# Kernel optimization log

Measured on AMD Instinct MI355X. Metric: run time of the kernel, lower is better.

The kernel has to match this reference:

```python
import jax, jax.numpy as jnp
import numpy as np

L, H, HD = 2, 8, 256
B, SP, SS = 2, 1024, 256
DP, DE = 2048, 1024
FP, FE = 8192, 4096
S = SP + SS


def setup_inputs() -> dict:
    key = jax.random.key(0)
    ks = iter(jax.random.split(key, 40))

    def w(shape):
        return jax.random.normal(next(ks), shape, jnp.float32) * (shape[-2] ** -0.5)

    inp = {
        "emb_p": jax.random.normal(next(ks), (B, SP, DP), jnp.float32),
        "emb_e": jax.random.normal(next(ks), (B, SS, DE), jnp.float32),
        "cond_p": jax.random.normal(next(ks), (B, DP), jnp.float32),
        "cond_e": jax.random.normal(next(ks), (B, DE), jnp.float32),
        "p_ada1": w((L, DP, 2 * DP)),
        "p_ada2": w((L, DP, 2 * DP)),
        "p_adaF": w((DP, 2 * DP)),
        "p_wq": w((L, DP, H * HD)),
        "p_wk": w((L, DP, H * HD)),
        "p_wv": w((L, DP, H * HD)),
        "p_wo": w((L, H * HD, DP)),
        "p_wg": w((L, DP, FP)),
        "p_wu": w((L, DP, FP)),
        "p_wd": w((L, FP, DP)),
        "e_ada1": w((L, DE, 2 * DE)),
        "e_ada2": w((L, DE, 2 * DE)),
        "e_adaF": w((DE, 2 * DE)),
        "e_wq": w((L, DE, H * HD)),
        "e_wk": w((L, DE, H * HD)),
        "e_wv": w((L, DE, H * HD)),
        "e_wo": w((L, H * HD, DE)),
        "e_wg": w((L, DE, FE)),
        "e_wu": w((L, DE, FE)),
        "e_wd": w((L, FE, DE)),
        "position_ids": jnp.broadcast_to(jnp.arange(S, dtype=jnp.int32)[None], (B, S)),
        "attn_mask": jnp.ones((B, S, S), dtype=bool),
    }
    return inp


def _rms(x):
    return x * jax.lax.rsqrt(jnp.mean(x * x, axis=-1, keepdims=True) + 1e-6)


def _ada(x, cond, W):
    # AdaRMS: cond -> (scale, gate); normed = rms(x) * (1 + scale)
    scale, gate = jnp.split(cond @ W, 2, axis=-1)  # each [B, D]
    return _rms(x) * (1.0 + scale)[:, None, :], gate[:, None, :]


def _rot_half(x):
    a, b = jnp.split(x, 2, axis=-1)
    return jnp.concatenate([-b, a], axis=-1)


def _forward(emb_p, emb_e, cond_p, cond_e,
             p_ada1, p_ada2, p_adaF, p_wq, p_wk, p_wv, p_wo, p_wg, p_wu, p_wd,
             e_ada1, e_ada2, e_adaF, e_wq, e_wk, e_wv, e_wo, e_wg, e_wu, e_wd,
             position_ids, attn_mask):
    # RoPE tables [B, 1, S, HD]
    inv = 1.0 / (10000.0 ** (jnp.arange(0, HD, 2, dtype=jnp.float32) / HD))
    fr = position_ids.astype(jnp.float32)[..., None] * inv  # [B, S, HD/2]
    ang = jnp.concatenate([fr, fr], axis=-1)
    cos, sin = jnp.cos(ang)[:, None], jnp.sin(ang)[:, None]
    bias = jnp.where(attn_mask[:, None], 0.0, jnp.finfo(jnp.float32).min)  # [B,1,S,S]
    scaling = HD ** -0.5

    xs = [emb_p, emb_e]
    conds = [cond_p, cond_e]
    prm = [
        dict(a1=p_ada1, a2=p_ada2, wq=p_wq, wk=p_wk, wv=p_wv, wo=p_wo, wg=p_wg, wu=p_wu, wd=p_wd),
        dict(a1=e_ada1, a2=e_ada2, wq=e_wq, wk=e_wk, wv=e_wv, wo=e_wo, wg=e_wg, wu=e_wu, wd=e_wd),
    ]
    seq_lens = [SP, SS]

    def heads(y):
        return y.reshape(B, -1, H, HD).transpose(0, 2, 1, 3)

    for l in range(L):
        qs, ksl, vs, gates = [], [], [], []
        for i in range(2):
            p = prm[i]
            h, g = _ada(xs[i], conds[i], p["a1"][l])
            gates.append(g)
            qs.append(heads(h @ p["wq"][l]))
            ksl.append(heads(h @ p["wk"][l]))
            vs.append(heads(h @ p["wv"][l]))
        # joint streams concatenated along sequence
        q = jnp.concatenate(qs, axis=2)   # [B,H,S,HD]
        k = jnp.concatenate(ksl, axis=2)
        v = jnp.concatenate(vs, axis=2)
        q = q * cos + _rot_half(q) * sin
        k = k * cos + _rot_half(k) * sin
        scores = jnp.einsum("bhqd,bhkd->bhqk", q, k) * scaling + bias
        probs = jax.nn.softmax(scores, axis=-1)
        att = jnp.einsum("bhqk,bhkd->bhqd", probs, v)
        att = att.transpose(0, 2, 1, 3).reshape(B, S, H * HD)
        start = 0
        for i in range(2):
            p = prm[i]
            end = start + seq_lens[i]
            o = att[:, start:end] @ p["wo"][l]
            x = xs[i] + o * gates[i]                 # gated attention residual
            res = x
            h2, g2 = _ada(x, conds[i], p["a2"][l])
            m = (jax.nn.gelu(h2 @ p["wg"][l], approximate=True) * (h2 @ p["wu"][l])) @ p["wd"][l]
            xs[i] = res + m * g2                     # gated MLP residual
            start = end
    out_p, _ = _ada(xs[0], cond_p, p_adaF)
    out_e, _ = _ada(xs[1], cond_e, e_adaF)
    return out_p, out_e


def reference(emb_p, emb_e, cond_p, cond_e,
              p_ada1, p_ada2, p_adaF, p_wq, p_wk, p_wv, p_wo, p_wg, p_wu, p_wd,
              e_ada1, e_ada2, e_adaF, e_wq, e_wk, e_wv, e_wo, e_wg, e_wu, e_wd,
              position_ids, attn_mask):
    return _forward(emb_p, emb_e, cond_p, cond_e,
                    p_ada1, p_ada2, p_adaF, p_wq, p_wk, p_wv, p_wo, p_wg, p_wu, p_wd,
                    e_ada1, e_ada2, e_adaF, e_wq, e_wk, e_wv, e_wo, e_wg, e_wu, e_wd,
                    position_ids, attn_mask)
```

## Files before the change

### kernel.cpp

```cpp
#include <hip/hip_runtime.h>
#include <math.h>

namespace {

constexpr int NL = 2, NH = 8, DH = 256;
constexpr int NB = 2, SEQP = 1024, SEQS = 256, SEQ = SEQP + SEQS;
constexpr int DIMP = 2048, DIME = 1024, FFP = 8192, FFE = 4096;
constexpr int HH = NH * DH;
constexpr int QKVN = 3 * HH;

typedef __attribute__((ext_vector_type(8))) short bf16x8;
typedef __attribute__((ext_vector_type(4))) float f32x4;

__device__ inline ushort f2b(float f) {
  union { float f; unsigned u; } x{f};
  unsigned r = (x.u + 0x7FFFu + ((x.u >> 16) & 1u)) >> 16;
  return (ushort)r;
}
__device__ inline float b2f(ushort u) {
  union { unsigned u; float f; } x{(unsigned)u << 16};
  return x.f;
}
__device__ inline void stv(float* p, float v) { *p = v; }
__device__ inline void stv(ushort* p, float v) { *p = f2b(v); }

__device__ inline void gld16(const void* g, void* l) {
  __builtin_amdgcn_global_load_lds(
      (const __attribute__((address_space(1))) void*)g,
      (__attribute__((address_space(3))) void*)l, 16, 0, 0);
}


__global__ void copy4_k(float4* __restrict__ dst, const float4* __restrict__ src) {
  long i = (long)blockIdx.x * blockDim.x + threadIdx.x;
  dst[i] = src[i];
}

__global__ void rope_tab_k(const int* __restrict__ pos, float* __restrict__ cosb,
                           float* __restrict__ sinb) {
  long bs = blockIdx.x;
  int d = threadIdx.x;
  int i = d & (DH / 2 - 1);
  float inv = expf(-(2.0f * (float)i / (float)DH) * logf(10000.0f));
  float ang = (float)pos[bs] * inv;
  cosb[bs * DH + d] = cosf(ang);
  sinb[bs * DH + d] = sinf(ang);
}

__global__ __launch_bounds__(256) void ada_k(const float* __restrict__ cond,
    const float* __restrict__ W, float* __restrict__ part, int D, int twoD) {
  __shared__ float lc[2 * 2048];
  int t = threadIdx.x;
  int j = blockIdx.x * 256 + t;
  int chunk = blockIdx.y;
  int cl = D / gridDim.y;
  int d0 = chunk * cl;
  for (int i = t; i < 2 * D; i += 256) lc[i] = cond[i];
  __syncthreads();
  float a0 = 0.f, a1 = 0.f;
  for (int d = d0; d < d0 + cl; ++d) {
    float wvv = W[(long)d * twoD + j];
    a0 = fmaf(lc[d], wvv, a0);
    a1 = fmaf(lc[D + d], wvv, a1);
  }
  part[((long)chunk * 2 + 0) * twoD + j] = a0;
  part[((long)chunk * 2 + 1) * twoD + j] = a1;
}

__global__ void ada_red_k(const float* __restrict__ part, float* __restrict__ sg,
                          int twoD, int nch) {
  int idx = blockIdx.x * 256 + threadIdx.x;
  int b = idx / twoD, j = idx - b * twoD;
  float s = 0.f;
  for (int c = 0; c < nch; ++c) s += part[((long)c * 2 + b) * twoD + j];
  sg[(long)b * twoD + j] = s;
}

template <typename OT>
__global__ __launch_bounds__(256) void rms_k(const float* __restrict__ x,
    const float* __restrict__ sg, OT* __restrict__ out, int D, int rowsPerB) {
  long row = blockIdx.x;
  int b = (int)(row / rowsPerB);
  const float* xr = x + row * (long)D;
  OT* po = out + row * (long)D;
  const float* sc = sg + (long)b * 2 * D;
  int t = threadIdx.x;
  float ss = 0.f;
  for (int i = t; i < D; i += 256) { float v = xr[i]; ss = fmaf(v, v, ss); }
  for (int o = 32; o; o >>= 1) ss += __shfl_xor(ss, o);
  __shared__ float wr[4];
  if ((t & 63) == 0) wr[t >> 6] = ss;
  __syncthreads();
  float rs = rsqrtf((wr[0] + wr[1] + wr[2] + wr[3]) / (float)D + 1e-6f);
  for (int i = t; i < D; i += 256) stv(po + i, xr[i] * rs * (1.f + sc[i]));
}

__global__ void gated_add_k(float* __restrict__ x, const float* __restrict__ y,
                            const float* __restrict__ g, int D, int rowsPerB) {
  long idx = (long)blockIdx.x * 256 + threadIdx.x;
  int d = (int)(idx % D);
  int b = (int)(idx / ((long)rowsPerB * D));
  x[idx] = fmaf(y[idx], g[(long)b * 2 * D + d], x[idx]);
}

__global__ __launch_bounds__(256) void wconv_k(const float* __restrict__ in,
    ushort* __restrict__ out, int N, int K) {
  __shared__ float tile[64][65];
  int n0 = blockIdx.x << 6, k0 = blockIdx.y << 6;
  int t = threadIdx.x, r = t >> 4, c4 = (t & 15) << 2;
#pragma unroll
  for (int rr = 0; rr < 64; rr += 16) {
    float4 v = *(const float4*)(in + (long)(k0 + r + rr) * N + n0 + c4);
    tile[r + rr][c4 + 0] = v.x; tile[r + rr][c4 + 1] = v.y;
    tile[r + rr][c4 + 2] = v.z; tile[r + rr][c4 + 3] = v.w;
  }
  __syncthreads();
#pragma unroll
  for (int rr = 0; rr < 64; rr += 16) {
    int n = r + rr;
    ushort4 o;
    o.x = f2b(tile[c4 + 0][n]); o.y = f2b(tile[c4 + 1][n]);
    o.z = f2b(tile[c4 + 2][n]); o.w = f2b(tile[c4 + 3][n]);
    *(ushort4*)(out + (long)(n0 + n) * K + k0 + c4) = o;
  }
}

__global__ __launch_bounds__(256) void rope_qk_k(const ushort* __restrict__ qkv,
    const float* __restrict__ cosb, const float* __restrict__ sinb,
    ushort* __restrict__ qj, ushort* __restrict__ kj, int Si, int ofs) {
  long bs = blockIdx.x;
  int b = (int)(bs / Si), s = (int)(bs % Si);
  int c = blockIdx.y * 256 + threadIdx.x;
  int h = c >> 8, hd = c & 255;
  long tin = bs * (long)QKVN;
  float q = b2f(qkv[tin + c]), k = b2f(qkv[tin + HH + c]);
  float qp = b2f(qkv[tin + (c ^ 128)]), kp = b2f(qkv[tin + HH + (c ^ 128)]);
  long sgi = ((long)b * SEQ + ofs + s) * DH + hd;
  float cv = cosb[sgi], sv = sinb[sgi];
  float qr = (hd < 128) ? -qp : qp, kr = (hd < 128) ? -kp : kp;
  long o = (((long)b * NH + h) * SEQ + ofs + s) * (long)DH + hd;
  qj[o] = f2b(fmaf(q, cv, qr * sv));
  kj[o] = f2b(fmaf(k, cv, kr * sv));
}

__global__ __launch_bounds__(256) void vtrans_k(const ushort* __restrict__ qkv,
    ushort* __restrict__ vjT, int Si, int ofs) {
  __shared__ ushort tile[64][80];
  int z = blockIdx.z, b = z >> 3, h = z & 7;
  int s0 = blockIdx.x << 6, d0 = blockIdx.y << 6;
  int t = threadIdx.x, r = t >> 3, c8 = (t & 7) << 3;
#pragma unroll
  for (int rr = 0; rr < 64; rr += 32) {
    const ushort* src = qkv + (long)(b * Si + s0 + r + rr) * QKVN + 2 * HH + h * DH + d0 + c8;
    *(uint4*)&tile[r + rr][c8] = *(const uint4*)src;
  }
  __syncthreads();
#pragma unroll
  for (int rr = 0; rr < 64; rr += 32) {
    int drow = r + rr;
    ushort o[8];
#pragma unroll
    for (int j = 0; j < 8; ++j) o[j] = tile[c8 + j][drow];
    *(uint4*)(vjT + ((long)(b * NH + h) * DH + d0 + drow) * SEQ + ofs + s0 + c8) =
        *(const uint4*)o;
  }
}

__global__ __launch_bounds__(256) void softmax_k(float* __restrict__ scores) {
  float* p = scores + (long)blockIdx.y * SEQ * SEQ + (long)blockIdx.x * SEQ;
  ushort* po = (ushort*)p;
  int t = threadIdx.x;
  float v[5];
  float mx = -3.4e38f;
#pragma unroll
  for (int i = 0; i < 5; ++i) { v[i] = p[t + i * 256] * 0.0625f; mx = fmaxf(mx, v[i]); }
  for (int o = 32; o; o >>= 1) mx = fmaxf(mx, __shfl_xor(mx, o));
  __shared__ float wr[4];
  if ((t & 63) == 0) wr[t >> 6] = mx;
  __syncthreads();
  mx = fmaxf(fmaxf(wr[0], wr[1]), fmaxf(wr[2], wr[3]));
  __syncthreads();
  float s = 0.f;
#pragma unroll
  for (int i = 0; i < 5; ++i) { v[i] = expf(v[i] - mx); s += v[i]; }
  for (int o = 32; o; o >>= 1) s += __shfl_xor(s, o);
  if ((t & 63) == 0) wr[t >> 6] = s;
  __syncthreads();
  float inv = 1.f / (wr[0] + wr[1] + wr[2] + wr[3]);
#pragma unroll
  for (int i = 0; i < 5; ++i) po[t + i * 256] = f2b(v[i] * inv);
}

__global__ __launch_bounds__(256) void gelumul_k(const ushort* __restrict__ in,
    ushort* __restrict__ out, int F) {
  long v = (long)blockIdx.x * 256 + threadIdx.x;
  int fv = F >> 3;
  long m = v / fv; int f8 = (int)(v % fv) << 3;
  const ushort* gp = in + m * 2 * F + f8;
  uint4 gv = *(const uint4*)gp;
  uint4 uv = *(const uint4*)(gp + F);
  const ushort* gs = (const ushort*)&gv;
  const ushort* us = (const ushort*)&uv;
  ushort ov[8];
#pragma unroll
  for (int j = 0; j < 8; ++j) {
    float g = b2f(gs[j]);
    float ge = 0.5f * g * (1.f + tanhf(0.7978845608028654f * fmaf(0.044715f * g, g * g, g)));
    ov[j] = f2b(ge * b2f(us[j]));
  }
  *(uint4*)(out + m * F + f8) = *(const uint4*)ov;
}

__global__ void redsum_k(const float4* __restrict__ in, float4* __restrict__ out,
                         long MN4, int ns) {
  long i = (long)blockIdx.x * 256 + threadIdx.x;
  float4 s = in[i];
  for (int c = 1; c < ns; ++c) {
    float4 v = in[(long)c * MN4 + i];
    s.x += v.x; s.y += v.y; s.z += v.z; s.w += v.w;
  }
  out[i] = s;
}

template <int EPI>
__global__ __launch_bounds__(256) void bgemm_k(
    const ushort* __restrict__ A, const ushort* __restrict__ B,
    float* __restrict__ Cf, ushort* __restrict__ Cb, int K,
    int lda, int ldb, int ldc,
    long sA1, long sA2, long sB1, long sB2, long sC1, long sC2, int bdiv) {
  __shared__ ushort As[128 * 32];
  __shared__ ushort Bs[128 * 32];
  int t = threadIdx.x;
  int z = blockIdx.z, z1 = z / bdiv, z2 = z % bdiv;
  A += z1 * sA1 + z2 * sA2;
  B += z1 * sB1 + z2 * sB2;
  long cofs = z1 * sC1 + z2 * sC2;
  int m0 = blockIdx.y * 128, n0 = blockIdx.x * 128;
  int srow = t >> 2, scol = (t & 3) << 3;
  const ushort* gA0 = A + (long)(m0 + srow) * lda + scol;
  const ushort* gA1 = A + (long)(m0 + srow + 64) * lda + scol;
  const ushort* gB0 = B + (long)(n0 + srow) * ldb + scol;
  const ushort* gB1 = B + (long)(n0 + srow + 64) * ldb + scol;
  ushort* lA0 = &As[srow * 32 + scol];
  ushort* lA1 = &As[(srow + 64) * 32 + scol];
  ushort* lB0 = &Bs[srow * 32 + scol];
  ushort* lB1 = &Bs[(srow + 64) * 32 + scol];
  int lane = t & 63;
  int wm = ((t >> 6) & 1) << 6, wn = (t >> 7) << 6;
  int fr = lane & 15, fk = (lane >> 4) << 3;
  f32x4 acc[4][4] = {};
  for (int k0 = 0; k0 < K; k0 += 32) {
    if (k0) __syncthreads();
    gld16(gA0 + k0, lA0);
    gld16(gA1 + k0, lA1);
    gld16(gB0 + k0, lB0);
    gld16(gB1 + k0, lB1);
    __syncthreads();
    bf16x8 a[4], b[4];
#pragma unroll
    for (int m = 0; m < 4; ++m)
      a[m] = *(const bf16x8*)&As[(wm + m * 16 + fr) * 32 + fk];
#pragma unroll
    for (int n = 0; n < 4; ++n)
      b[n] = *(const bf16x8*)&Bs[(wn + n * 16 + fr) * 32 + fk];
#pragma unroll
    for (int m = 0; m < 4; ++m)
#pragma unroll
      for (int n = 0; n < 4; ++n)
        acc[m][n] = __builtin_amdgcn_mfma_f32_16x16x32_bf16(a[m], b[n], acc[m][n], 0, 0, 0);
  }
  int cr = (lane >> 4) << 2, cc = lane & 15;
#pragma unroll
  for (int m = 0; m < 4; ++m) {
    int row = m0 + wm + m * 16 + cr;
#pragma unroll
    for (int n = 0; n < 4; ++n) {
      int col = n0 + wn + n * 16 + cc;
#pragma unroll
      for (int r = 0; r < 4; ++r) {
        long idx = cofs + (long)(row + r) * ldc + col;
        if (EPI == 0) Cf[idx] = acc[m][n][r];
        else Cb[idx] = f2b(acc[m][n][r]);
      }
    }
  }
}

template <int EPI>
__global__ __launch_bounds__(512, 2) void bgemm256_k(
    const ushort* __restrict__ A, const ushort* __restrict__ B,
    float* __restrict__ Cf, ushort* __restrict__ Cb, int K,
    int lda, int ldb, int ldc,
    long sA1, long sA2, long sB1, long sB2, long sC1, long sC2, int bdiv) {
  __shared__ ushort As[4][256 * 32];
  __shared__ ushort Bs[4][256 * 32];
  int t = threadIdx.x;
  int z = blockIdx.z, z1 = z / bdiv, z2 = z % bdiv;
  A += z1 * sA1 + z2 * sA2;
  B += z1 * sB1 + z2 * sB2;
  long cofs = z1 * sC1 + z2 * sC2;
  int nx = gridDim.x;
  int nwg = nx * gridDim.y;
  int wg = blockIdx.y * nx + blockIdx.x;
  int q = nwg >> 3, r = nwg & 7;
  int xcd = wg & 7, wi = wg >> 3;
  int swz = (xcd < r ? xcd * (q + 1) : r * (q + 1) + (xcd - r) * q) + wi;
  int n0 = (swz % nx) << 8;
  int m0 = (swz / nx) << 8;

  int srow = t >> 2;
  int gc = ((t & 3) ^ ((srow >> 1) & 3)) << 3;
  const ushort* ga0 = A + (long)(m0 + srow) * lda + gc;
  const ushort* ga1 = A + (long)(m0 + 128 + srow) * lda + gc;
  const ushort* gb0 = B + (long)(n0 + srow) * ldb + gc;
  const ushort* gb1 = B + (long)(n0 + 128 + srow) * ldb + gc;

  int lane = t & 63, wid = t >> 6;
  int wm = wid >> 2, wn = wid & 3;
  int fr = lane & 15, sl = lane >> 4;

  int aoff[8], boff[4];
#pragma unroll
  for (int m = 0; m < 8; ++m) {
    int row = wm * 128 + m * 16 + fr;
    aoff[m] = row * 32 + ((sl ^ ((row >> 1) & 3)) << 3);
  }
#pragma unroll
  for (int n = 0; n < 4; ++n) {
    int row = wn * 64 + n * 16 + fr;
    boff[n] = row * 32 + ((sl ^ ((row >> 1) & 3)) << 3);
  }

  f32x4 acc[8][4] = {};
  int nt = K >> 5;

#define STAGE(ti) { int b_ = (ti) & 3; int k_ = (ti) << 5;        \
    gld16(ga0 + k_, &As[b_][t * 8]);                              \
    gld16(ga1 + k_, &As[b_][4096 + t * 8]);                       \
    gld16(gb0 + k_, &Bs[b_][t * 8]);                              \
    gld16(gb1 + k_, &Bs[b_][4096 + t * 8]); }

  STAGE(0); STAGE(1); STAGE(2);
  for (int ti = 0; ti < nt; ++ti) {
    if (ti + 2 < nt)      asm volatile("s_waitcnt vmcnt(8)" ::: "memory");
    else if (ti + 1 < nt) asm volatile("s_waitcnt vmcnt(4)" ::: "memory");
    else                  asm volatile("s_waitcnt vmcnt(0)" ::: "memory");
    __builtin_amdgcn_s_barrier();
    if (ti + 3 < nt) STAGE(ti + 3);
    int bu = ti & 3;
    bf16x8 av[8], bv[4];
#pragma unroll
    for (int m = 0; m < 8; ++m) av[m] = *(const bf16x8*)&As[bu][aoff[m]];
#pragma unroll
    for (int n = 0; n < 4; ++n) bv[n] = *(const bf16x8*)&Bs[bu][boff[n]];
    __builtin_amdgcn_s_setprio(1);
#pragma unroll
    for (int m = 0; m < 8; ++m)
#pragma unroll
      for (int n = 0; n < 4; ++n)
        acc[m][n] = __builtin_amdgcn_mfma_f32_16x16x32_bf16(av[m], bv[n], acc[m][n], 0, 0, 0);
    __builtin_amdgcn_s_setprio(0);
  }
#undef STAGE

  int cr = sl << 2, cc = fr;
#pragma unroll
  for (int m = 0; m < 8; ++m) {
    int row = m0 + wm * 128 + m * 16 + cr;
#pragma unroll
    for (int n = 0; n < 4; ++n) {
      int col = n0 + wn * 64 + n * 16 + cc;
#pragma unroll
      for (int rr = 0; rr < 4; ++rr) {
        long idx = cofs + (long)(row + rr) * ldc + col;
        if (EPI == 0) Cf[idx] = acc[m][n][rr];
        else Cb[idx] = f2b(acc[m][n][rr]);
      }
    }
  }
}

}

extern "C" void kernel_launch(void* const* d_in, const int* in_sizes, int n_in,
                              void* d_out, int out_size, void* d_ws, size_t ws_size,
                              hipStream_t stream) {
  (void)in_sizes; (void)n_in; (void)out_size;
  const float* emb_p = (const float*)d_in[0];
  const float* emb_e = (const float*)d_in[1];
  const float* cond[2] = {(const float*)d_in[2], (const float*)d_in[3]};
  const float* ada1[2] = {(const float*)d_in[4], (const float*)d_in[14]};
  const float* ada2[2] = {(const float*)d_in[5], (const float*)d_in[15]};
  const float* adaF[2] = {(const float*)d_in[6], (const float*)d_in[16]};
  const float* wq[2] = {(const float*)d_in[7], (const float*)d_in[17]};
  const float* wk[2] = {(const float*)d_in[8], (const float*)d_in[18]};
  const float* wv[2] = {(const float*)d_in[9], (const float*)d_in[19]};
  const float* wo[2] = {(const float*)d_in[10], (const float*)d_in[20]};
  const float* wg[2] = {(const float*)d_in[11], (const float*)d_in[21]};
  const float* wu[2] = {(const float*)d_in[12], (const float*)d_in[22]};
  const float* wd[2] = {(const float*)d_in[13], (const float*)d_in[23]};
  const int* pos = (const int*)d_in[24];

  const int Ds[2] = {DIMP, DIME};
  const int Fs[2] = {FFP, FFE};
  const int Sis[2] = {SEQP, SEQS};
  const int ofss[2] = {0, SEQP};

  char* base = (char*)d_ws;
  size_t off = 0;
  auto alF = [&](size_t n) { float* r = (float*)(base + off); off += (n * 4 + 255) & ~(size_t)255; return r; };
  auto alH = [&](size_t n) { ushort* r = (ushort*)(base + off); off += (n * 2 + 255) & ~(size_t)255; return r; };

  float* xs[2]; ushort* hb[2]; float* sg[2];
  xs[0] = alF((size_t)NB * SEQP * DIMP);
  xs[1] = alF((size_t)NB * SEQS * DIME);
  float* cosb = alF((size_t)NB * SEQ * DH);
  float* sinb = alF((size_t)NB * SEQ * DH);
  sg[0] = alF((size_t)NB * 2 * DIMP);
  sg[1] = alF((size_t)NB * 2 * DIME);
  float* part = alF((size_t)8 * 2 * 2 * DIMP);
  float* tmp = alF((size_t)NB * SEQP * DIMP);
  float* scores = alF((size_t)NB * NH * SEQ * SEQ);
  hb[0] = alH((size_t)NB * SEQP * DIMP);
  hb[1] = alH((size_t)NB * SEQS * DIME);
  ushort* qkvt = alH((size_t)NB * SEQP * QKVN);
  ushort* qj = alH((size_t)NB * NH * SEQ * DH);
  ushort* kj = alH((size_t)NB * NH * SEQ * DH);
  ushort* vjT = alH((size_t)NB * NH * DH * SEQ);
  ushort* att2b = alH((size_t)NB * SEQ * HH);
  ushort* wT = alH((size_t)2 * FFP * DIMP);
  if (off > ws_size) return;

  float* pbuf = scores;
  ushort* ffb2 = (ushort*)scores;
  ushort* ffb = (ushort*)((char*)scores + (size_t)70 * 1024 * 1024);

  copy4_k<<<(NB * SEQP * DIMP / 4) / 256, 256, 0, stream>>>((float4*)xs[0], (const float4*)emb_p);
  copy4_k<<<(NB * SEQS * DIME / 4) / 256, 256, 0, stream>>>((float4*)xs[1], (const float4*)emb_e);
  rope_tab_k<<<NB * SEQ, DH, 0, stream>>>(pos, cosb, sinb);

  for (int l = 0; l < NL; ++l) {
    for (int i = 0; i < 2; ++i) {
      int D = Ds[i], Si = Sis[i], M = NB * Si;
      const float* a1 = ada1[i] + (size_t)l * D * 2 * D;
      ada_k<<<dim3(2 * D / 256, 8), 256, 0, stream>>>(cond[i], a1, part, D, 2 * D);
      ada_red_k<<<4 * D / 256, 256, 0, stream>>>(part, sg[i], 2 * D, 8);
      rms_k<ushort><<<M, 256, 0, stream>>>(xs[i], sg[i], hb[i], D, Si);
      const float* W3[3] = {wq[i] + (size_t)l * D * HH, wk[i] + (size_t)l * D * HH,
                            wv[i] + (size_t)l * D * HH};
      for (int j = 0; j < 3; ++j)
        wconv_k<<<dim3(HH / 64, D / 64), 256, 0, stream>>>(W3[j], wT + (size_t)j * HH * D, HH, D);
      if (i == 0)
        bgemm256_k<1><<<dim3(QKVN / 256, M / 256, 1), 512, 0, stream>>>(
            hb[i], wT, nullptr, qkvt, D, D, D, QKVN, 0, 0, 0, 0, 0, 0, 1);
      else
        bgemm_k<1><<<dim3(QKVN / 128, M / 128, 1), 256, 0, stream>>>(
            hb[i], wT, nullptr, qkvt, D, D, D, QKVN, 0, 0, 0, 0, 0, 0, 1);
      rope_qk_k<<<dim3(M, HH / 256), 256, 0, stream>>>(qkvt, cosb, sinb, qj, kj, Si, ofss[i]);
      vtrans_k<<<dim3(Si / 64, DH / 64, NB * NH), 256, 0, stream>>>(qkvt, vjT, Si, ofss[i]);
    }
    bgemm256_k<0><<<dim3(SEQ / 256, SEQ / 256, NB * NH), 512, 0, stream>>>(
        qj, kj, scores, nullptr, DH, DH, DH, SEQ,
        (long)SEQ * DH, 0, (long)SEQ * DH, 0, (long)SEQ * SEQ, 0, 1);
    softmax_k<<<dim3(SEQ, NB * NH), 256, 0, stream>>>(scores);
    bgemm_k<1><<<dim3(DH / 128, SEQ / 128, NB * NH), 256, 0, stream>>>(
        (const ushort*)scores, vjT, nullptr, att2b, SEQ, 2 * SEQ, SEQ, HH,
        (long)2 * NH * SEQ * SEQ, (long)2 * SEQ * SEQ,
        (long)NH * DH * SEQ, (long)DH * SEQ,
        (long)SEQ * HH, (long)DH, NH);
    for (int i = 0; i < 2; ++i) {
      int D = Ds[i], F = Fs[i], Si = Sis[i], M = NB * Si;
      wconv_k<<<dim3(D / 64, HH / 64), 256, 0, stream>>>(wo[i] + (size_t)l * HH * D, wT, D, HH);
      if (i == 0)
        bgemm256_k<0><<<dim3(D / 256, Si / 256, NB * 4), 512, 0, stream>>>(
            att2b, wT, pbuf, nullptr, 512, HH, HH, D,
            (long)SEQ * HH, 512, 0, 512, (long)Si * D, (long)M * D, 4);
      else
        bgemm_k<0><<<dim3(D / 128, Si / 128, NB * 4), 256, 0, stream>>>(
            att2b + (size_t)ofss[i] * HH, wT, pbuf, nullptr, 512, HH, HH, D,
            (long)SEQ * HH, 512, 0, 512, (long)Si * D, (long)M * D, 4);
      redsum_k<<<M * D / 4 / 256, 256, 0, stream>>>((const float4*)pbuf, (float4*)tmp,
                                                    (long)M * D / 4, 4);
      gated_add_k<<<M * D / 256, 256, 0, stream>>>(xs[i], tmp, sg[i] + D, D, Si);
      const float* a2 = ada2[i] + (size_t)l * D * 2 * D;
      ada_k<<<dim3(2 * D / 256, 8), 256, 0, stream>>>(cond[i], a2, part, D, 2 * D);
      ada_red_k<<<4 * D / 256, 256, 0, stream>>>(part, sg[i], 2 * D, 8);
      rms_k<ushort><<<M, 256, 0, stream>>>(xs[i], sg[i], hb[i], D, Si);
      wconv_k<<<dim3(F / 64, D / 64), 256, 0, stream>>>(wg[i] + (size_t)l * D * F, wT, F, D);
      wconv_k<<<dim3(F / 64, D / 64), 256, 0, stream>>>(wu[i] + (size_t)l * D * F,
                                                        wT + (size_t)F * D, F, D);
      if (i == 0)
        bgemm256_k<1><<<dim3(2 * F / 256, M / 256, 1), 512, 0, stream>>>(
            hb[i], wT, nullptr, ffb2, D, D, D, 2 * F, 0, 0, 0, 0, 0, 0, 1);
      else
        bgemm_k<1><<<dim3(2 * F / 128, M / 128, 1), 256, 0, stream>>>(
            hb[i], wT, nullptr, ffb2, D, D, D, 2 * F, 0, 0, 0, 0, 0, 0, 1);
      gelumul_k<<<(long)M * F / 8 / 256, 256, 0, stream>>>(ffb2, ffb, F);
      wconv_k<<<dim3(D / 64, F / 64), 256, 0, stream>>>(wd[i] + (size_t)l * F * D, wT, D, F);
      if (i == 0)
        bgemm256_k<0><<<dim3(D / 256, M / 256, 4), 512, 0, stream>>>(
            ffb, wT, pbuf, nullptr, F / 4, F, F, D,
            0, F / 4, 0, F / 4, 0, (long)M * D, 4);
      else
        bgemm_k<0><<<dim3(D / 128, M / 128, 8), 256, 0, stream>>>(
            ffb, wT, pbuf, nullptr, F / 8, F, F, D,
            0, F / 8, 0, F / 8, 0, (long)M * D, 8);
      redsum_k<<<M * D / 4 / 256, 256, 0, stream>>>((const float4*)pbuf, (float4*)tmp,
                                                    (long)M * D / 4, i == 0 ? 4 : 8);
      gated_add_k<<<M * D / 256, 256, 0, stream>>>(xs[i], tmp, sg[i] + D, D, Si);
    }
  }
  float* outp = (float*)d_out;
  for (int i = 0; i < 2; ++i) {
    int D = Ds[i], Si = Sis[i];
    ada_k<<<dim3(2 * D / 256, 8), 256, 0, stream>>>(cond[i], adaF[i], part, D, 2 * D);
    ada_red_k<<<4 * D / 256, 256, 0, stream>>>(part, sg[i], 2 * D, 8);
    rms_k<float><<<NB * Si, 256, 0, stream>>>(xs[i], sg[i], outp, D, Si);
    outp += (size_t)NB * Si * D;
  }
}
```

Measured before the change: 2.433 ms.

## Rework 256-tile GEMM into 8-phase ping-pong pipeline and fuse split-K reduction

Replaces the 4-stage, 32-wide-K pipelined 256x256 GEMM with a double-buffered 64-wide-K kernel. Each K step is split into eight phases that interleave LDS reads, async global-to-LDS loads and MFMA quadrants with barriers. The goal is to hide load latency and keep more MFMA work per sync. It also switches the tile order to column-major and fuses the split-K reduction into the gated residual add, which removes a separate pass and its temporary buffer. The extra barriers per phase add sync overhead and could hurt if the schedule does not overlap well.

```diff
diff --git a/kernel.cpp b/kernel.cpp
--- a/kernel.cpp
+++ b/kernel.cpp
@@ -95,12 +95,15 @@
   for (int i = t; i < D; i += 256) stv(po + i, xr[i] * rs * (1.f + sc[i]));
 }
 
-__global__ void gated_add_k(float* __restrict__ x, const float* __restrict__ y,
-                            const float* __restrict__ g, int D, int rowsPerB) {
+__global__ void gared_k(float* __restrict__ x, const float* __restrict__ part,
+                        const float* __restrict__ g, int D, int rowsPerB,
+                        long MN, int ns) {
   long idx = (long)blockIdx.x * 256 + threadIdx.x;
   int d = (int)(idx % D);
   int b = (int)(idx / ((long)rowsPerB * D));
-  x[idx] = fmaf(y[idx], g[(long)b * 2 * D + d], x[idx]);
+  float s = part[idx];
+  for (int c = 1; c < ns; ++c) s += part[(long)c * MN + idx];
+  x[idx] = fmaf(s, g[(long)b * 2 * D + d], x[idx]);
 }
 
 __global__ __launch_bounds__(256) void wconv_k(const float* __restrict__ in,
@@ -209,17 +212,6 @@
     ov[j] = f2b(ge * b2f(us[j]));
   }
   *(uint4*)(out + m * F + f8) = *(const uint4*)ov;
-}
-
-__global__ void redsum_k(const float4* __restrict__ in, float4* __restrict__ out,
-                         long MN4, int ns) {
-  long i = (long)blockIdx.x * 256 + threadIdx.x;
-  float4 s = in[i];
-  for (int c = 1; c < ns; ++c) {
-    float4 v = in[(long)c * MN4 + i];
-    s.x += v.x; s.y += v.y; s.z += v.z; s.w += v.w;
-  }
-  out[i] = s;
 }
 
 template <int EPI>
@@ -287,81 +279,123 @@
 }
 
 template <int EPI>
-__global__ __launch_bounds__(512, 2) void bgemm256_k(
+__global__ __launch_bounds__(512, 2) void bgemm8_k(
     const ushort* __restrict__ A, const ushort* __restrict__ B,
     float* __restrict__ Cf, ushort* __restrict__ Cb, int K,
     int lda, int ldb, int ldc,
     long sA1, long sA2, long sB1, long sB2, long sC1, long sC2, int bdiv) {
-  __shared__ ushort As[4][256 * 32];
-  __shared__ ushort Bs[4][256 * 32];
+  __shared__ ushort As[2][2][256 * 32];
+  __shared__ ushort Bs[2][2][256 * 32];
   int t = threadIdx.x;
   int z = blockIdx.z, z1 = z / bdiv, z2 = z % bdiv;
   A += z1 * sA1 + z2 * sA2;
   B += z1 * sB1 + z2 * sB2;
   long cofs = z1 * sC1 + z2 * sC2;
-  int nx = gridDim.x;
-  int nwg = nx * gridDim.y;
-  int wg = blockIdx.y * nx + blockIdx.x;
-  int q = nwg >> 3, r = nwg & 7;
+  int gy = gridDim.y, nwg = gridDim.x * gy;
+  int wg = blockIdx.y * gridDim.x + blockIdx.x;
+  int q8 = nwg >> 3, r8 = nwg & 7;
   int xcd = wg & 7, wi = wg >> 3;
-  int swz = (xcd < r ? xcd * (q + 1) : r * (q + 1) + (xcd - r) * q) + wi;
-  int n0 = (swz % nx) << 8;
-  int m0 = (swz / nx) << 8;
+  int swz = (xcd < r8 ? xcd * (q8 + 1) : r8 * (q8 + 1) + (xcd - r8) * q8) + wi;
+  int m0 = (swz % gy) << 8;
+  int n0 = (swz / gy) << 8;
 
   int srow = t >> 2;
-  int gc = ((t & 3) ^ ((srow >> 1) & 3)) << 3;
-  const ushort* ga0 = A + (long)(m0 + srow) * lda + gc;
-  const ushort* ga1 = A + (long)(m0 + 128 + srow) * lda + gc;
-  const ushort* gb0 = B + (long)(n0 + srow) * ldb + gc;
-  const ushort* gb1 = B + (long)(n0 + 128 + srow) * ldb + gc;
+  int scol = ((t & 3) ^ ((srow >> 1) & 3)) << 3;
+  const ushort* ga = A + (long)(m0 + srow) * lda + scol;
+  const ushort* gb = B + (long)(n0 + srow) * ldb + scol;
+  long a128 = (long)128 * lda, b128 = (long)128 * ldb;
 
   int lane = t & 63, wid = t >> 6;
   int wm = wid >> 2, wn = wid & 3;
   int fr = lane & 15, sl = lane >> 4;
 
-  int aoff[8], boff[4];
-#pragma unroll
-  for (int m = 0; m < 8; ++m) {
-    int row = wm * 128 + m * 16 + fr;
-    aoff[m] = row * 32 + ((sl ^ ((row >> 1) & 3)) << 3);
-  }
-#pragma unroll
-  for (int n = 0; n < 4; ++n) {
-    int row = wn * 64 + n * 16 + fr;
-    boff[n] = row * 32 + ((sl ^ ((row >> 1) & 3)) << 3);
+  int ao[2][4], bo[4];
+#pragma unroll
+  for (int mq = 0; mq < 2; ++mq)
+#pragma unroll
+    for (int mi = 0; mi < 4; ++mi) {
+      int row = wm * 128 + mq * 64 + mi * 16 + fr;
+      ao[mq][mi] = row * 32 + ((sl ^ ((row >> 1) & 3)) << 3);
+    }
+#pragma unroll
+  for (int nf = 0; nf < 4; ++nf) {
+    int row = wn * 64 + nf * 16 + fr;
+    bo[nf] = row * 32 + ((sl ^ ((row >> 1) & 3)) << 3);
   }
 
   f32x4 acc[8][4] = {};
-  int nt = K >> 5;
-
-#define STAGE(ti) { int b_ = (ti) & 3; int k_ = (ti) << 5;        \
-    gld16(ga0 + k_, &As[b_][t * 8]);                              \
-    gld16(ga1 + k_, &As[b_][4096 + t * 8]);                       \
-    gld16(gb0 + k_, &Bs[b_][t * 8]);                              \
-    gld16(gb1 + k_, &Bs[b_][4096 + t * 8]); }
-
-  STAGE(0); STAGE(1); STAGE(2);
-  for (int ti = 0; ti < nt; ++ti) {
-    if (ti + 2 < nt)      asm volatile("s_waitcnt vmcnt(8)" ::: "memory");
-    else if (ti + 1 < nt) asm volatile("s_waitcnt vmcnt(4)" ::: "memory");
-    else                  asm volatile("s_waitcnt vmcnt(0)" ::: "memory");
-    __builtin_amdgcn_s_barrier();
-    if (ti + 3 < nt) STAGE(ti + 3);
-    int bu = ti & 3;
-    bf16x8 av[8], bv[4];
-#pragma unroll
-    for (int m = 0; m < 8; ++m) av[m] = *(const bf16x8*)&As[bu][aoff[m]];
-#pragma unroll
-    for (int n = 0; n < 4; ++n) bv[n] = *(const bf16x8*)&Bs[bu][boff[n]];
-    __builtin_amdgcn_s_setprio(1);
-#pragma unroll
-    for (int m = 0; m < 8; ++m)
-#pragma unroll
-      for (int n = 0; n < 4; ++n)
-        acc[m][n] = __builtin_amdgcn_mfma_f32_16x16x32_bf16(av[m], bv[n], acc[m][n], 0, 0, 0);
-    __builtin_amdgcn_s_setprio(0);
-  }
-#undef STAGE
+  int nkt = K >> 6;
+
+#define STGA(kt, kw) { const ushort* s_ = ga + ((long)(kt) << 6) + ((kw) << 5); \
+    gld16(s_, &As[(kt) & 1][kw][t * 8]);                                        \
+    gld16(s_ + a128, &As[(kt) & 1][kw][4096 + t * 8]); }
+#define STGB(kt, kw) { const ushort* s_ = gb + ((long)(kt) << 6) + ((kw) << 5); \
+    gld16(s_, &Bs[(kt) & 1][kw][t * 8]);                                        \
+    gld16(s_ + b128, &Bs[(kt) & 1][kw][4096 + t * 8]); }
+
+  STGA(0, 0); STGA(0, 1); STGB(0, 0); STGB(0, 1);
+  if (nkt > 1) STGA(1, 0);
+  asm volatile("s_waitcnt vmcnt(2)" ::: "memory");
+  __builtin_amdgcn_s_barrier();
+  __builtin_amdgcn_sched_barrier(0);
+
+  bf16x8 a[4][2], b[4][2];
+  for (int it = 0; it < nkt; it += 2) {
+#pragma unroll
+    for (int p = 0; p < 8; ++p) {
+      const int buf = p >> 2;
+      const int q = p & 3, mq = q >> 1, nq = q & 1;
+      if (q == 0) {
+#pragma unroll
+        for (int x = 0; x < 4; ++x) {
+          a[x][0] = *(const bf16x8*)&As[buf][0][ao[0][x]];
+          a[x][1] = *(const bf16x8*)&As[buf][1][ao[0][x]];
+        }
+#pragma unroll
+        for (int nf = 0; nf < 4; ++nf) {
+          b[nf][0] = *(const bf16x8*)&Bs[buf][0][bo[nf]];
+          b[nf][1] = *(const bf16x8*)&Bs[buf][1][bo[nf]];
+        }
+      } else if (q == 2) {
+#pragma unroll
+        for (int x = 0; x < 4; ++x) {
+          a[x][0] = *(const bf16x8*)&As[buf][0][ao[1][x]];
+          a[x][1] = *(const bf16x8*)&As[buf][1][ao[1][x]];
+        }
+      }
+      if (p == 0) { STGA(it + 1, 1); }
+      else if (p == 1) { STGB(it + 1, 0); }
+      else if (p == 2) { STGB(it + 1, 1); }
+      else if (p == 3) {
+        if (it + 2 < nkt) { STGA(it + 2, 0);
+          asm volatile("s_waitcnt vmcnt(2)" ::: "memory");
+        } else asm volatile("s_waitcnt vmcnt(0)" ::: "memory");
+      }
+      else if (p == 4) { if (it + 2 < nkt) STGA(it + 2, 1); }
+      else if (p == 5) { if (it + 2 < nkt) STGB(it + 2, 0); }
+      else if (p == 6) { if (it + 2 < nkt) STGB(it + 2, 1); }
+      else {
+        if (it + 3 < nkt) { STGA(it + 3, 0);
+          asm volatile("s_waitcnt vmcnt(2)" ::: "memory");
+        } else asm volatile("s_waitcnt vmcnt(0)" ::: "memory");
+      }
+      __builtin_amdgcn_s_barrier();
+      if (p == 3 || p == 7) __builtin_amdgcn_sched_barrier(0);
+      __builtin_amdgcn_s_setprio(1);
+#pragma unroll
+      for (int mi = 0; mi < 4; ++mi)
+#pragma unroll
+        for (int ni = 0; ni < 2; ++ni)
+#pragma unroll
+          for (int kw = 0; kw < 2; ++kw)
+            acc[mq * 4 + mi][nq * 2 + ni] = __builtin_amdgcn_mfma_f32_16x16x32_bf16(
+                a[mi][kw], b[nq * 2 + ni][kw], acc[mq * 4 + mi][nq * 2 + ni], 0, 0, 0);
+      __builtin_amdgcn_s_setprio(0);
+      __builtin_amdgcn_s_barrier();
+    }
+  }
+#undef STGA
+#undef STGB
 
   int cr = sl << 2, cc = fr;
 #pragma unroll
@@ -419,7 +453,6 @@
   sg[0] = alF((size_t)NB * 2 * DIMP);
   sg[1] = alF((size_t)NB * 2 * DIME);
   float* part = alF((size_t)8 * 2 * 2 * DIMP);
-  float* tmp = alF((size_t)NB * SEQP * DIMP);
   float* scores = alF((size_t)NB * NH * SEQ * SEQ);
   hb[0] = alH((size_t)NB * SEQP * DIMP);
   hb[1] = alH((size_t)NB * SEQS * DIME);
@@ -451,7 +484,7 @@
       for (int j = 0; j < 3; ++j)
         wconv_k<<<dim3(HH / 64, D / 64), 256, 0, stream>>>(W3[j], wT + (size_t)j * HH * D, HH, D);
       if (i == 0)
-        bgemm256_k<1><<<dim3(QKVN / 256, M / 256, 1), 512, 0, stream>>>(
+        bgemm8_k<1><<<dim3(QKVN / 256, M / 256, 1), 512, 0, stream>>>(
             hb[i], wT, nullptr, qkvt, D, D, D, QKVN, 0, 0, 0, 0, 0, 0, 1);
       else
         bgemm_k<1><<<dim3(QKVN / 128, M / 128, 1), 256, 0, stream>>>(
@@ -459,7 +492,7 @@
       rope_qk_k<<<dim3(M, HH / 256), 256, 0, stream>>>(qkvt, cosb, sinb, qj, kj, Si, ofss[i]);
       vtrans_k<<<dim3(Si / 64, DH / 64, NB * NH), 256, 0, stream>>>(qkvt, vjT, Si, ofss[i]);
     }
-    bgemm256_k<0><<<dim3(SEQ / 256, SEQ / 256, NB * NH), 512, 0, stream>>>(
+    bgemm8_k<0><<<dim3(SEQ / 256, SEQ / 256, NB * NH), 512, 0, stream>>>(
         qj, kj, scores, nullptr, DH, DH, DH, SEQ,
         (long)SEQ * DH, 0, (long)SEQ * DH, 0, (long)SEQ * SEQ, 0, 1);
     softmax_k<<<dim3(SEQ, NB * NH), 256, 0, stream>>>(scores);
@@ -472,16 +505,15 @@
       int D = Ds[i], F = Fs[i], Si = Sis[i], M = NB * Si;
       wconv_k<<<dim3(D / 64, HH / 64), 256, 0, stream>>>(wo[i] + (size_t)l * HH * D, wT, D, HH);
       if (i == 0)
-        bgemm256_k<0><<<dim3(D / 256, Si / 256, NB * 4), 512, 0, stream>>>(
+        bgemm8_k<0><<<dim3(D / 256, Si / 256, NB * 4), 512, 0, stream>>>(
             att2b, wT, pbuf, nullptr, 512, HH, HH, D,
             (long)SEQ * HH, 512, 0, 512, (long)Si * D, (long)M * D, 4);
       else
         bgemm_k<0><<<dim3(D / 128, Si / 128, NB * 4), 256, 0, stream>>>(
             att2b + (size_t)ofss[i] * HH, wT, pbuf, nullptr, 512, HH, HH, D,
             (long)SEQ * HH, 512, 0, 512, (long)Si * D, (long)M * D, 4);
-      redsum_k<<<M * D / 4 / 256, 256, 0, stream>>>((const float4*)pbuf, (float4*)tmp,
-                                                    (long)M * D / 4, 4);
-      gated_add_k<<<M * D / 256, 256, 0, stream>>>(xs[i], tmp, sg[i] + D, D, Si);
+      gared_k<<<M * D / 256, 256, 0, stream>>>(xs[i], pbuf, sg[i] + D, D, Si,
+                                               (long)M * D, 4);
       const float* a2 = ada2[i] + (size_t)l * D * 2 * D;
       ada_k<<<dim3(2 * D / 256, 8), 256, 0, stream>>>(cond[i], a2, part, D, 2 * D);
       ada_red_k<<<4 * D / 256, 256, 0, stream>>>(part, sg[i], 2 * D, 8);
@@ -490,7 +522,7 @@
       wconv_k<<<dim3(F / 64, D / 64), 256, 0, stream>>>(wu[i] + (size_t)l * D * F,
                                                         wT + (size_t)F * D, F, D);
       if (i == 0)
-        bgemm256_k<1><<<dim3(2 * F / 256, M / 256, 1), 512, 0, stream>>>(
+        bgemm8_k<1><<<dim3(2 * F / 256, M / 256, 1), 512, 0, stream>>>(
             hb[i], wT, nullptr, ffb2, D, D, D, 2 * F, 0, 0, 0, 0, 0, 0, 1);
       else
         bgemm_k<1><<<dim3(2 * F / 128, M / 128, 1), 256, 0, stream>>>(
@@ -498,16 +530,15 @@
       gelumul_k<<<(long)M * F / 8 / 256, 256, 0, stream>>>(ffb2, ffb, F);
       wconv_k<<<dim3(D / 64, F / 64), 256, 0, stream>>>(wd[i] + (size_t)l * F * D, wT, D, F);
       if (i == 0)
-        bgemm256_k<0><<<dim3(D / 256, M / 256, 4), 512, 0, stream>>>(
+        bgemm8_k<0><<<dim3(D / 256, M / 256, 4), 512, 0, stream>>>(
             ffb, wT, pbuf, nullptr, F / 4, F, F, D,
             0, F / 4, 0, F / 4, 0, (long)M * D, 4);
       else
         bgemm_k<0><<<dim3(D / 128, M / 128, 8), 256, 0, stream>>>(
             ffb, wT, pbuf, nullptr, F / 8, F, F, D,
             0, F / 8, 0, F / 8, 0, (long)M * D, 8);
-      redsum_k<<<M * D / 4 / 256, 256, 0, stream>>>((const float4*)pbuf, (float4*)tmp,
-                                                    (long)M * D / 4, i == 0 ? 4 : 8);
-      gated_add_k<<<M * D / 256, 256, 0, stream>>>(xs[i], tmp, sg[i] + D, D, Si);
+      gared_k<<<M * D / 256, 256, 0, stream>>>(xs[i], pbuf, sg[i] + D, D, Si,
+                                               (long)M * D, i == 0 ? 4 : 8);
     }
   }
   float* outp = (float*)d_out;
```

Result: faster. 2.208 ms (-9.2%).

## Split 256-tile GEMM mainloop into two half-phases, fuse split-K reduce with gated residual

Applied to the files above, without the earlier changes.

The 256x256 GEMM now loads A and B tiles separately with a two-deep prefetch instead of three. Each K step runs as two half-phases of MFMAs over the A rows, with a barrier between them, so the B load for step ti+2 goes out mid-step. The workgroup swizzle now walks M first instead of N, which changes which tiles share an XCD for L2 reuse. The separate split-K reduction kernel and gated-add kernel are merged into one kernel that sums the partials and applies the gate, removing a temporary buffer and one launch plus its memory round trip. The extra barrier per step and the shallower prefetch could expose more memory latency.

```diff
diff --git a/kernel.cpp b/kernel.cpp
--- a/kernel.cpp
+++ b/kernel.cpp
@@ -95,12 +95,15 @@
   for (int i = t; i < D; i += 256) stv(po + i, xr[i] * rs * (1.f + sc[i]));
 }
 
-__global__ void gated_add_k(float* __restrict__ x, const float* __restrict__ y,
-                            const float* __restrict__ g, int D, int rowsPerB) {
+__global__ void gared_k(float* __restrict__ x, const float* __restrict__ part,
+                        const float* __restrict__ g, int D, int rowsPerB,
+                        long MN, int ns) {
   long idx = (long)blockIdx.x * 256 + threadIdx.x;
   int d = (int)(idx % D);
   int b = (int)(idx / ((long)rowsPerB * D));
-  x[idx] = fmaf(y[idx], g[(long)b * 2 * D + d], x[idx]);
+  float s = part[idx];
+  for (int c = 1; c < ns; ++c) s += part[(long)c * MN + idx];
+  x[idx] = fmaf(s, g[(long)b * 2 * D + d], x[idx]);
 }
 
 __global__ __launch_bounds__(256) void wconv_k(const float* __restrict__ in,
@@ -209,17 +212,6 @@
     ov[j] = f2b(ge * b2f(us[j]));
   }
   *(uint4*)(out + m * F + f8) = *(const uint4*)ov;
-}
-
-__global__ void redsum_k(const float4* __restrict__ in, float4* __restrict__ out,
-                         long MN4, int ns) {
-  long i = (long)blockIdx.x * 256 + threadIdx.x;
-  float4 s = in[i];
-  for (int c = 1; c < ns; ++c) {
-    float4 v = in[(long)c * MN4 + i];
-    s.x += v.x; s.y += v.y; s.z += v.z; s.w += v.w;
-  }
-  out[i] = s;
 }
 
 template <int EPI>
@@ -287,7 +279,7 @@
 }
 
 template <int EPI>
-__global__ __launch_bounds__(512, 2) void bgemm256_k(
+__global__ __launch_bounds__(512, 2) void bgemm8_k(
     const ushort* __restrict__ A, const ushort* __restrict__ B,
     float* __restrict__ Cf, ushort* __restrict__ Cb, int K,
     int lda, int ldb, int ldc,
@@ -299,21 +291,20 @@
   A += z1 * sA1 + z2 * sA2;
   B += z1 * sB1 + z2 * sB2;
   long cofs = z1 * sC1 + z2 * sC2;
-  int nx = gridDim.x;
-  int nwg = nx * gridDim.y;
-  int wg = blockIdx.y * nx + blockIdx.x;
-  int q = nwg >> 3, r = nwg & 7;
+  int gy = gridDim.y, nwg = gridDim.x * gy;
+  int wg = blockIdx.y * gridDim.x + blockIdx.x;
+  int q8 = nwg >> 3, r8 = nwg & 7;
   int xcd = wg & 7, wi = wg >> 3;
-  int swz = (xcd < r ? xcd * (q + 1) : r * (q + 1) + (xcd - r) * q) + wi;
-  int n0 = (swz % nx) << 8;
-  int m0 = (swz / nx) << 8;
+  int swz = (xcd < r8 ? xcd * (q8 + 1) : r8 * (q8 + 1) + (xcd - r8) * q8) + wi;
+  int m0 = (swz % gy) << 8;
+  int n0 = (swz / gy) << 8;
 
   int srow = t >> 2;
-  int gc = ((t & 3) ^ ((srow >> 1) & 3)) << 3;
-  const ushort* ga0 = A + (long)(m0 + srow) * lda + gc;
-  const ushort* ga1 = A + (long)(m0 + 128 + srow) * lda + gc;
-  const ushort* gb0 = B + (long)(n0 + srow) * ldb + gc;
-  const ushort* gb1 = B + (long)(n0 + 128 + srow) * ldb + gc;
+  int scol = ((t & 3) ^ ((srow >> 1) & 3)) << 3;
+  const ushort* ga0 = A + (long)(m0 + srow) * lda + scol;
+  const ushort* ga1 = A + (long)(m0 + 128 + srow) * lda + scol;
+  const ushort* gb0 = B + (long)(n0 + srow) * ldb + scol;
+  const ushort* gb1 = B + (long)(n0 + 128 + srow) * ldb + scol;
 
   int lane = t & 63, wid = t >> 6;
   int wm = wid >> 2, wn = wid & 3;
@@ -334,34 +325,54 @@
   f32x4 acc[8][4] = {};
   int nt = K >> 5;
 
-#define STAGE(ti) { int b_ = (ti) & 3; int k_ = (ti) << 5;        \
-    gld16(ga0 + k_, &As[b_][t * 8]);                              \
-    gld16(ga1 + k_, &As[b_][4096 + t * 8]);                       \
-    gld16(gb0 + k_, &Bs[b_][t * 8]);                              \
+#define STGA(ti) { int b_ = (ti) & 3; int k_ = (ti) << 5;  \
+    gld16(ga0 + k_, &As[b_][t * 8]);                       \
+    gld16(ga1 + k_, &As[b_][4096 + t * 8]); }
+#define STGB(ti) { int b_ = (ti) & 3; int k_ = (ti) << 5;  \
+    gld16(gb0 + k_, &Bs[b_][t * 8]);                       \
     gld16(gb1 + k_, &Bs[b_][4096 + t * 8]); }
 
-  STAGE(0); STAGE(1); STAGE(2);
+  STGA(0); STGB(0);
+  if (nt > 1) { STGA(1); STGB(1); }
+
   for (int ti = 0; ti < nt; ++ti) {
-    if (ti + 2 < nt)      asm volatile("s_waitcnt vmcnt(8)" ::: "memory");
-    else if (ti + 1 < nt) asm volatile("s_waitcnt vmcnt(4)" ::: "memory");
-    else                  asm volatile("s_waitcnt vmcnt(0)" ::: "memory");
-    __builtin_amdgcn_s_barrier();
-    if (ti + 3 < nt) STAGE(ti + 3);
     int bu = ti & 3;
-    bf16x8 av[8], bv[4];
-#pragma unroll
-    for (int m = 0; m < 8; ++m) av[m] = *(const bf16x8*)&As[bu][aoff[m]];
+    if (ti + 2 < nt) {
+      STGA(ti + 2);
+      asm volatile("s_waitcnt vmcnt(6)" ::: "memory");
+    } else if (ti + 1 < nt) {
+      asm volatile("s_waitcnt vmcnt(4)" ::: "memory");
+    } else {
+      asm volatile("s_waitcnt vmcnt(0)" ::: "memory");
+    }
+    asm volatile("s_barrier" ::: "memory");
+    bf16x8 av[4], bv[4];
+#pragma unroll
+    for (int m = 0; m < 4; ++m) av[m] = *(const bf16x8*)&As[bu][aoff[m]];
 #pragma unroll
     for (int n = 0; n < 4; ++n) bv[n] = *(const bf16x8*)&Bs[bu][boff[n]];
     __builtin_amdgcn_s_setprio(1);
 #pragma unroll
-    for (int m = 0; m < 8; ++m)
+    for (int m = 0; m < 4; ++m)
 #pragma unroll
       for (int n = 0; n < 4; ++n)
         acc[m][n] = __builtin_amdgcn_mfma_f32_16x16x32_bf16(av[m], bv[n], acc[m][n], 0, 0, 0);
     __builtin_amdgcn_s_setprio(0);
-  }
-#undef STAGE
+    if (ti + 2 < nt) STGB(ti + 2);
+    asm volatile("s_barrier" ::: "memory");
+    bf16x8 aw[4];
+#pragma unroll
+    for (int m = 0; m < 4; ++m) aw[m] = *(const bf16x8*)&As[bu][aoff[4 + m]];
+    __builtin_amdgcn_s_setprio(1);
+#pragma unroll
+    for (int m = 0; m < 4; ++m)
+#pragma unroll
+      for (int n = 0; n < 4; ++n)
+        acc[4 + m][n] = __builtin_amdgcn_mfma_f32_16x16x32_bf16(aw[m], bv[n], acc[4 + m][n], 0, 0, 0);
+    __builtin_amdgcn_s_setprio(0);
+  }
+#undef STGA
+#undef STGB
 
   int cr = sl << 2, cc = fr;
 #pragma unroll
@@ -419,7 +430,6 @@
   sg[0] = alF((size_t)NB * 2 * DIMP);
   sg[1] = alF((size_t)NB * 2 * DIME);
   float* part = alF((size_t)8 * 2 * 2 * DIMP);
-  float* tmp = alF((size_t)NB * SEQP * DIMP);
   float* scores = alF((size_t)NB * NH * SEQ * SEQ);
   hb[0] = alH((size_t)NB * SEQP * DIMP);
   hb[1] = alH((size_t)NB * SEQS * DIME);
@@ -451,7 +461,7 @@
       for (int j = 0; j < 3; ++j)
         wconv_k<<<dim3(HH / 64, D / 64), 256, 0, stream>>>(W3[j], wT + (size_t)j * HH * D, HH, D);
       if (i == 0)
-        bgemm256_k<1><<<dim3(QKVN / 256, M / 256, 1), 512, 0, stream>>>(
+        bgemm8_k<1><<<dim3(QKVN / 256, M / 256, 1), 512, 0, stream>>>(
             hb[i], wT, nullptr, qkvt, D, D, D, QKVN, 0, 0, 0, 0, 0, 0, 1);
       else
         bgemm_k<1><<<dim3(QKVN / 128, M / 128, 1), 256, 0, stream>>>(
@@ -459,7 +469,7 @@
       rope_qk_k<<<dim3(M, HH / 256), 256, 0, stream>>>(qkvt, cosb, sinb, qj, kj, Si, ofss[i]);
       vtrans_k<<<dim3(Si / 64, DH / 64, NB * NH), 256, 0, stream>>>(qkvt, vjT, Si, ofss[i]);
     }
-    bgemm256_k<0><<<dim3(SEQ / 256, SEQ / 256, NB * NH), 512, 0, stream>>>(
+    bgemm8_k<0><<<dim3(SEQ / 256, SEQ / 256, NB * NH), 512, 0, stream>>>(
         qj, kj, scores, nullptr, DH, DH, DH, SEQ,
         (long)SEQ * DH, 0, (long)SEQ * DH, 0, (long)SEQ * SEQ, 0, 1);
     softmax_k<<<dim3(SEQ, NB * NH), 256, 0, stream>>>(scores);
@@ -472,16 +482,15 @@
       int D = Ds[i], F = Fs[i], Si = Sis[i], M = NB * Si;
       wconv_k<<<dim3(D / 64, HH / 64), 256, 0, stream>>>(wo[i] + (size_t)l * HH * D, wT, D, HH);
       if (i == 0)
-        bgemm256_k<0><<<dim3(D / 256, Si / 256, NB * 4), 512, 0, stream>>>(
+        bgemm8_k<0><<<dim3(D / 256, Si / 256, NB * 4), 512, 0, stream>>>(
             att2b, wT, pbuf, nullptr, 512, HH, HH, D,
             (long)SEQ * HH, 512, 0, 512, (long)Si * D, (long)M * D, 4);
       else
         bgemm_k<0><<<dim3(D / 128, Si / 128, NB * 4), 256, 0, stream>>>(
             att2b + (size_t)ofss[i] * HH, wT, pbuf, nullptr, 512, HH, HH, D,
             (long)SEQ * HH, 512, 0, 512, (long)Si * D, (long)M * D, 4);
-      redsum_k<<<M * D / 4 / 256, 256, 0, stream>>>((const float4*)pbuf, (float4*)tmp,
-                                                    (long)M * D / 4, 4);
-      gated_add_k<<<M * D / 256, 256, 0, stream>>>(xs[i], tmp, sg[i] + D, D, Si);
+      gared_k<<<M * D / 256, 256, 0, stream>>>(xs[i], pbuf, sg[i] + D, D, Si,
+                                               (long)M * D, 4);
       const float* a2 = ada2[i] + (size_t)l * D * 2 * D;
       ada_k<<<dim3(2 * D / 256, 8), 256, 0, stream>>>(cond[i], a2, part, D, 2 * D);
       ada_red_k<<<4 * D / 256, 256, 0, stream>>>(part, sg[i], 2 * D, 8);
@@ -490,7 +499,7 @@
       wconv_k<<<dim3(F / 64, D / 64), 256, 0, stream>>>(wu[i] + (size_t)l * D * F,
                                                         wT + (size_t)F * D, F, D);
       if (i == 0)
-        bgemm256_k<1><<<dim3(2 * F / 256, M / 256, 1), 512, 0, stream>>>(
+        bgemm8_k<1><<<dim3(2 * F / 256, M / 256, 1), 512, 0, stream>>>(
             hb[i], wT, nullptr, ffb2, D, D, D, 2 * F, 0, 0, 0, 0, 0, 0, 1);
       else
         bgemm_k<1><<<dim3(2 * F / 128, M / 128, 1), 256, 0, stream>>>(
@@ -498,16 +507,15 @@
       gelumul_k<<<(long)M * F / 8 / 256, 256, 0, stream>>>(ffb2, ffb, F);
       wconv_k<<<dim3(D / 64, F / 64), 256, 0, stream>>>(wd[i] + (size_t)l * F * D, wT, D, F);
       if (i == 0)
-        bgemm256_k<0><<<dim3(D / 256, M / 256, 4), 512, 0, stream>>>(
+        bgemm8_k<0><<<dim3(D / 256, M / 256, 4), 512, 0, stream>>>(
             ffb, wT, pbuf, nullptr, F / 4, F, F, D,
             0, F / 4, 0, F / 4, 0, (long)M * D, 4);
       else
         bgemm_k<0><<<dim3(D / 128, M / 128, 8), 256, 0, stream>>>(
             ffb, wT, pbuf, nullptr, F / 8, F, F, D,
             0, F / 8, 0, F / 8, 0, (long)M * D, 8);
-      redsum_k<<<M * D / 4 / 256, 256, 0, stream>>>((const float4*)pbuf, (float4*)tmp,
-                                                    (long)M * D / 4, i == 0 ? 4 : 8);
-      gated_add_k<<<M * D / 256, 256, 0, stream>>>(xs[i], tmp, sg[i] + D, D, Si);
+      gared_k<<<M * D / 256, 256, 0, stream>>>(xs[i], pbuf, sg[i] + D, D, Si,
+                                               (long)M * D, i == 0 ? 4 : 8);
     }
   }
   float* outp = (float*)d_out;
```

Result: faster. 2.240 ms (-7.9%).
